# Kernel tuning notes

Measured on AMD Instinct MI355X. Metric: run time of the kernel, lower is better.

Reference implementation:

```python
import jax, jax.numpy as jnp
import numpy as np

N, D_IN, D_OUT, E = 16384, 2048, 2048, 8


def setup_inputs() -> dict:
    key = jax.random.key(0)
    k1, k2, k3, k4 = jax.random.split(key, 4)
    x = jax.random.normal(k1, (N, D_IN), dtype=jnp.float32)
    idxs = jax.random.randint(k2, (N,), 0, E, dtype=jnp.int64)
    # nn.Linear params: weight [out, in], bias [out]; stacked over experts.
    W = jax.random.normal(k3, (E, D_OUT, D_IN), dtype=jnp.float32) * (1.0 / np.sqrt(D_IN))
    b = jax.random.normal(k4, (E, D_OUT), dtype=jnp.float32) * 0.01
    return {"x": x, "idxs": idxs, "W": W, "b": b}


def reference(x, idxs, W, b):
    # Hard-routed MoE: each token goes to exactly one expert's Linear, then ReLU.
    # Loop over the small fixed expert count; each iteration is one dense GEMM
    # over all tokens, combined with a per-token routing mask (equivalent math
    # to the original masked gather/scatter since every token matches exactly
    # one expert id in [0, E)).
    n_experts = W.shape[0]
    y = jnp.zeros((x.shape[0], W.shape[1]), dtype=x.dtype)
    for e in range(n_experts):
        mask = (idxs == e)[:, None]  # [N, 1]
        y_e = x @ W[e].T + b[e]      # [N, out]
        y = jnp.where(mask, y_e, y)
    return jax.nn.relu(y)
```

## Files before the change

kernel.cpp:

```cpp
#include <hip/hip_runtime.h>
#include <stdint.h>

#define N_TOK 16384
#define D_IN  2048
#define D_OUT 2048
#define NEXP  8

#define BM 256
#define BN 128
#define BK 32
#define NKT (D_IN / BK)
#define NX4 (N_TOK * D_IN / 4)
#define NW4 (NEXP * D_OUT * D_IN / 4)

typedef __attribute__((ext_vector_type(8))) short bf16x8;
typedef __attribute__((ext_vector_type(4))) float f32x4;
typedef __attribute__((ext_vector_type(4))) unsigned short u16x4;

static __device__ __forceinline__ unsigned short f2bf(float x) {
  unsigned u = __builtin_bit_cast(unsigned, x);
  u += 0x7FFFu + ((u >> 16) & 1u);
  return (unsigned short)(u >> 16);
}
static __device__ __forceinline__ float bf2f(unsigned short h) {
  unsigned u = ((unsigned)h) << 16;
  return __builtin_bit_cast(float, u);
}

__global__ void zero_cnt(int* cnt) {
  if (threadIdx.x < NEXP) cnt[threadIdx.x] = 0;
}

__global__ void route_kernel(const int* __restrict__ idxs, int* __restrict__ cnt,
                             int* __restrict__ bucket) {
  __shared__ int hist[NEXP];
  __shared__ int base[NEXP];
  __shared__ int pos[NEXP];
  const int t = blockIdx.x * 256 + threadIdx.x;
  if (threadIdx.x < NEXP) { hist[threadIdx.x] = 0; pos[threadIdx.x] = 0; }
  __syncthreads();
  const int e = idxs[t];
  atomicAdd(&hist[e], 1);
  __syncthreads();
  if (threadIdx.x < NEXP)
    base[threadIdx.x] = atomicAdd(&cnt[threadIdx.x], hist[threadIdx.x]);
  __syncthreads();
  const int r = atomicAdd(&pos[e], 1);
  bucket[e * N_TOK + base[e] + r] = t;
}

__global__ void split_both(const float* __restrict__ x, const float* __restrict__ W,
                           unsigned short* __restrict__ xhi, unsigned short* __restrict__ xlo,
                           unsigned short* __restrict__ whi, unsigned short* __restrict__ wlo) {
  const int total = NX4 + NW4;
  for (int i = blockIdx.x * blockDim.x + threadIdx.x; i < total; i += gridDim.x * blockDim.x) {
    const bool isx = (i < NX4);
    const int j = isx ? i : i - NX4;
    const float4 v = isx ? ((const float4*)x)[j] : ((const float4*)W)[j];
    float f[4] = {v.x, v.y, v.z, v.w};
    u16x4 h, l;
#pragma unroll
    for (int k = 0; k < 4; ++k) {
      unsigned short hh = f2bf(f[k]);
      h[k] = hh;
      l[k] = f2bf(f[k] - bf2f(hh));
    }
    unsigned short* dh = (isx ? xhi : whi) + (size_t)j * 4;
    unsigned short* dl = (isx ? xlo : wlo) + (size_t)j * 4;
    *(u16x4*)dh = h;
    *(u16x4*)dl = l;
  }
}

#define GLD16(g, l)                                                                    \
  __builtin_amdgcn_global_load_lds((const __attribute__((address_space(1))) void*)(g), \
                                   (__attribute__((address_space(3))) void*)(l), 16, 0, 0)
#define SB() __builtin_amdgcn_sched_barrier(0)
#define BAR() __builtin_amdgcn_s_barrier()

__global__ __launch_bounds__(512)
void moe_gemm(const unsigned short* __restrict__ xhi, const unsigned short* __restrict__ xlo,
              const unsigned short* __restrict__ whi, const unsigned short* __restrict__ wlo,
              const float* __restrict__ bias, const int* __restrict__ cnt,
              const int* __restrict__ bucket, float* __restrict__ out) {
  const int bid = blockIdx.x;
  const int e = bid & 7;
  const int rem = bid >> 3;
  const int my = rem >> 4;
  const int nb = rem & 15;
  const int count = cnt[e];
  const int m0 = my * BM;
  if (m0 >= count) return;
  const int n0 = nb * BN;

  __shared__ __align__(16) char sbuf[3][49152];
  __shared__ int rowtok[BM];

  const int tid = threadIdx.x;
  const int lane = tid & 63;
  const int w = tid >> 6;
  const int wrM = (w >> 1) * 64;
  const int wcN = (w & 1) * 64;

  if (tid < BM) {
    int r = m0 + tid;
    rowtok[tid] = bucket[e * N_TOK + (r < count ? r : count - 1)];
  }
  __syncthreads();

  const unsigned short* whiE = whi + (size_t)e * D_OUT * D_IN;
  const unsigned short* wloE = wlo + (size_t)e * D_OUT * D_IN;
  const unsigned short* srcb[6];
  {
    const int g = tid >> 3;
    const int c = (tid & 7) ^ (g & 7);
    const int half = c >> 2, kc = c & 3;
#pragma unroll
    for (int q = 0; q < 4; ++q) {
      const int tok = rowtok[q * 64 + g];
      srcb[q] = (half ? xlo : xhi) + (size_t)tok * D_IN + kc * 8;
    }
#pragma unroll
    for (int q = 0; q < 2; ++q) {
      srcb[4 + q] = (half ? wloE : whiE) + (size_t)(n0 + q * 64 + g) * D_IN + kc * 8;
    }
  }
  const int dstw = w * 1024;

  const int off0 = (lane & 15) * 128 + (((lane >> 4) ^ (lane & 7)) * 16);

  f32x4 acc[4][4];
#pragma unroll
  for (int i = 0; i < 4; ++i)
#pragma unroll
    for (int j = 0; j < 4; ++j) acc[i][j] = (f32x4)0.0f;

#pragma unroll
  for (int q = 0; q < 4; ++q) GLD16(srcb[q], sbuf[0] + q * 8192 + dstw);
#pragma unroll
  for (int q = 0; q < 2; ++q) GLD16(srcb[4 + q], sbuf[0] + 32768 + q * 8192 + dstw);
#pragma unroll
  for (int q = 0; q < 4; ++q) GLD16(srcb[q] + BK, sbuf[1] + q * 8192 + dstw);
#pragma unroll
  for (int q = 0; q < 2; ++q) GLD16(srcb[4 + q] + BK, sbuf[1] + 32768 + q * 8192 + dstw);
  SB();
  asm volatile("s_waitcnt vmcnt(6)" ::: "memory");
  BAR(); SB();

#define COMPUTE(rb)                                                              \
  {                                                                              \
    bf16x8 ah[4], al[4], bh[4], bl[4];                                           \
    _Pragma("unroll") for (int m = 0; m < 4; ++m) {                              \
      const char* p = (rb) + (wrM + m * 16) * 128;                               \
      ah[m] = *(const bf16x8*)(p + off0);                                        \
      al[m] = *(const bf16x8*)(p + (off0 ^ 64));                                 \
    }                                                                            \
    _Pragma("unroll") for (int n = 0; n < 4; ++n) {                              \
      const char* p = (rb) + 32768 + (wcN + n * 16) * 128;                       \
      bh[n] = *(const bf16x8*)(p + off0);                                        \
      bl[n] = *(const bf16x8*)(p + (off0 ^ 64));                                 \
    }                                                                            \
    __builtin_amdgcn_s_setprio(1);                                               \
    _Pragma("unroll") for (int m = 0; m < 4; ++m)                                \
    _Pragma("unroll") for (int n = 0; n < 4; ++n) {                              \
      f32x4 a = acc[m][n];                                                       \
      a = __builtin_amdgcn_mfma_f32_16x16x32_bf16(ah[m], bh[n], a, 0, 0, 0);     \
      a = __builtin_amdgcn_mfma_f32_16x16x32_bf16(ah[m], bl[n], a, 0, 0, 0);     \
      a = __builtin_amdgcn_mfma_f32_16x16x32_bf16(al[m], bh[n], a, 0, 0, 0);     \
      acc[m][n] = a;                                                             \
    }                                                                            \
    __builtin_amdgcn_s_setprio(0);                                               \
  }

  int i = 0;
  for (; i < NKT - 2; ++i) {
    const char* rb = sbuf[i % 3];
    char* wb = sbuf[(i + 2) % 3];
    const int kt = (i + 2) * BK;
#pragma unroll
    for (int q = 0; q < 4; ++q) GLD16(srcb[q] + kt, wb + q * 8192 + dstw);
#pragma unroll
    for (int q = 0; q < 2; ++q) GLD16(srcb[4 + q] + kt, wb + 32768 + q * 8192 + dstw);
    SB();
    COMPUTE(rb);
    SB();
    asm volatile("s_waitcnt vmcnt(6)" ::: "memory");
    BAR(); SB();
  }
  {
    const char* rb = sbuf[i % 3];
    COMPUTE(rb);
    SB();
    asm volatile("s_waitcnt vmcnt(0)" ::: "memory");
    BAR(); SB();
    ++i;
  }
  {
    const char* rb = sbuf[i % 3];
    COMPUTE(rb);
  }

  const int r16 = lane & 15;
  const int rb4 = (lane >> 4) * 4;
#pragma unroll
  for (int n = 0; n < 4; ++n) {
    const int gn = n0 + wcN + n * 16 + r16;
    const float bv = bias[e * D_OUT + gn];
#pragma unroll
    for (int m = 0; m < 4; ++m) {
      const int lr = wrM + m * 16 + rb4;
#pragma unroll
      for (int i2 = 0; i2 < 4; ++i2) {
        const int row = lr + i2;
        if (m0 + row < count) {
          out[(size_t)rowtok[row] * D_OUT + gn] = fmaxf(acc[m][n][i2] + bv, 0.0f);
        }
      }
    }
  }
#undef COMPUTE
}

__global__ void fallback_kernel(const float* __restrict__ x, const int* __restrict__ idxs,
                                const float* __restrict__ W, const float* __restrict__ b,
                                float* __restrict__ out) {
  const int row = blockIdx.y;
  const int col = blockIdx.x * 256 + threadIdx.x;
  const int e = idxs[row];
  const float4* xr = (const float4*)(x + (size_t)row * D_IN);
  const float4* wr = (const float4*)(W + ((size_t)e * D_OUT + col) * D_IN);
  float acc = 0.f;
  for (int k = 0; k < D_IN / 4; ++k) {
    float4 a = xr[k], w = wr[k];
    acc += a.x * w.x + a.y * w.y + a.z * w.z + a.w * w.w;
  }
  out[(size_t)row * D_OUT + col] = fmaxf(acc + b[e * D_OUT + col], 0.0f);
}

extern "C" void kernel_launch(void* const* d_in, const int* in_sizes, int n_in,
                              void* d_out, int out_size, void* d_ws, size_t ws_size,
                              hipStream_t stream) {
  const float* x = (const float*)d_in[0];
  const int* idxs = (const int*)d_in[1];
  const float* W = (const float*)d_in[2];
  const float* b = (const float*)d_in[3];
  float* out = (float*)d_out;

  size_t off = 0;
  auto alloc = [&](size_t bytes) {
    void* p = (char*)d_ws + off;
    off += (bytes + 255) & ~(size_t)255;
    return p;
  };
  int* cnt = (int*)alloc(NEXP * sizeof(int));
  int* bucket = (int*)alloc((size_t)NEXP * N_TOK * sizeof(int));
  unsigned short* xhi = (unsigned short*)alloc((size_t)N_TOK * D_IN * 2);
  unsigned short* xlo = (unsigned short*)alloc((size_t)N_TOK * D_IN * 2);
  unsigned short* whi = (unsigned short*)alloc((size_t)NEXP * D_OUT * D_IN * 2);
  unsigned short* wlo = (unsigned short*)alloc((size_t)NEXP * D_OUT * D_IN * 2);

  if (off > ws_size) {
    dim3 g(D_OUT / 256, N_TOK, 1);
    fallback_kernel<<<g, 256, 0, stream>>>(x, idxs, W, b, out);
    return;
  }

  zero_cnt<<<1, 64, 0, stream>>>(cnt);
  route_kernel<<<N_TOK / 256, 256, 0, stream>>>(idxs, cnt, bucket);
  split_both<<<2048, 256, 0, stream>>>(x, W, xhi, xlo, whi, wlo);

  const int nblk = NEXP * (N_TOK / BM) * (D_OUT / BN);
  moe_gemm<<<nblk, 512, 0, stream>>>(xhi, xlo, whi, wlo, b, cnt, bucket, out);
}
```

Before: 953.6 us.

## Enlarge GEMM tile to 256x256 and switch to double-buffered LDS pipeline

Doubles the N tile from 128 to 256 so each 256-row block of x is reused across twice as many output columns, halving redundant A-tile loads per output. Waves are rearranged into a 2x4 grid, each computing 128x64 in two M-halves with a 32-entry accumulator array. The triple-buffered prefetch-two-ahead pipeline becomes a double-buffered prefetch-one-ahead loop with extra barriers per iteration. This raises register and LDS pressure and gives less latency hiding in exchange for better data reuse.

```diff
diff --git a/kernel.cpp b/kernel.cpp
--- a/kernel.cpp
+++ b/kernel.cpp
@@ -7,7 +7,7 @@
 #define NEXP  8
 
 #define BM 256
-#define BN 128
+#define BN 256
 #define BK 32
 #define NKT (D_IN / BK)
 #define NX4 (N_TOK * D_IN / 4)
@@ -86,21 +86,21 @@
   const int bid = blockIdx.x;
   const int e = bid & 7;
   const int rem = bid >> 3;
-  const int my = rem >> 4;
-  const int nb = rem & 15;
+  const int my = rem >> 3;
+  const int nb = rem & 7;
   const int count = cnt[e];
   const int m0 = my * BM;
   if (m0 >= count) return;
   const int n0 = nb * BN;
 
-  __shared__ __align__(16) char sbuf[3][49152];
+  __shared__ __align__(16) char sbuf[2][65536];
   __shared__ int rowtok[BM];
 
   const int tid = threadIdx.x;
   const int lane = tid & 63;
   const int w = tid >> 6;
-  const int wrM = (w >> 1) * 64;
-  const int wcN = (w & 1) * 64;
+  const int wr = w >> 2;
+  const int wc = w & 3;
 
   if (tid < BM) {
     int r = m0 + tid;
@@ -110,7 +110,7 @@
 
   const unsigned short* whiE = whi + (size_t)e * D_OUT * D_IN;
   const unsigned short* wloE = wlo + (size_t)e * D_OUT * D_IN;
-  const unsigned short* srcb[6];
+  const unsigned short* srcb[8];
   {
     const int g = tid >> 3;
     const int c = (tid & 7) ^ (g & 7);
@@ -121,7 +121,7 @@
       srcb[q] = (half ? xlo : xhi) + (size_t)tok * D_IN + kc * 8;
     }
 #pragma unroll
-    for (int q = 0; q < 2; ++q) {
+    for (int q = 0; q < 4; ++q) {
       srcb[4 + q] = (half ? wloE : whiE) + (size_t)(n0 + q * 64 + g) * D_IN + kc * 8;
     }
   }
@@ -129,86 +129,74 @@
 
   const int off0 = (lane & 15) * 128 + (((lane >> 4) ^ (lane & 7)) * 16);
 
-  f32x4 acc[4][4];
-#pragma unroll
-  for (int i = 0; i < 4; ++i)
+  f32x4 acc[8][4];
+#pragma unroll
+  for (int i = 0; i < 8; ++i)
 #pragma unroll
     for (int j = 0; j < 4; ++j) acc[i][j] = (f32x4)0.0f;
 
 #pragma unroll
-  for (int q = 0; q < 4; ++q) GLD16(srcb[q], sbuf[0] + q * 8192 + dstw);
-#pragma unroll
-  for (int q = 0; q < 2; ++q) GLD16(srcb[4 + q], sbuf[0] + 32768 + q * 8192 + dstw);
-#pragma unroll
-  for (int q = 0; q < 4; ++q) GLD16(srcb[q] + BK, sbuf[1] + q * 8192 + dstw);
-#pragma unroll
-  for (int q = 0; q < 2; ++q) GLD16(srcb[4 + q] + BK, sbuf[1] + 32768 + q * 8192 + dstw);
-  SB();
-  asm volatile("s_waitcnt vmcnt(6)" ::: "memory");
-  BAR(); SB();
-
-#define COMPUTE(rb)                                                              \
-  {                                                                              \
-    bf16x8 ah[4], al[4], bh[4], bl[4];                                           \
-    _Pragma("unroll") for (int m = 0; m < 4; ++m) {                              \
-      const char* p = (rb) + (wrM + m * 16) * 128;                               \
-      ah[m] = *(const bf16x8*)(p + off0);                                        \
-      al[m] = *(const bf16x8*)(p + (off0 ^ 64));                                 \
-    }                                                                            \
-    _Pragma("unroll") for (int n = 0; n < 4; ++n) {                              \
-      const char* p = (rb) + 32768 + (wcN + n * 16) * 128;                       \
-      bh[n] = *(const bf16x8*)(p + off0);                                        \
-      bl[n] = *(const bf16x8*)(p + (off0 ^ 64));                                 \
-    }                                                                            \
-    __builtin_amdgcn_s_setprio(1);                                               \
-    _Pragma("unroll") for (int m = 0; m < 4; ++m)                                \
-    _Pragma("unroll") for (int n = 0; n < 4; ++n) {                              \
-      f32x4 a = acc[m][n];                                                       \
-      a = __builtin_amdgcn_mfma_f32_16x16x32_bf16(ah[m], bh[n], a, 0, 0, 0);     \
-      a = __builtin_amdgcn_mfma_f32_16x16x32_bf16(ah[m], bl[n], a, 0, 0, 0);     \
-      a = __builtin_amdgcn_mfma_f32_16x16x32_bf16(al[m], bh[n], a, 0, 0, 0);     \
-      acc[m][n] = a;                                                             \
-    }                                                                            \
-    __builtin_amdgcn_s_setprio(0);                                               \
-  }
-
-  int i = 0;
-  for (; i < NKT - 2; ++i) {
-    const char* rb = sbuf[i % 3];
-    char* wb = sbuf[(i + 2) % 3];
-    const int kt = (i + 2) * BK;
-#pragma unroll
-    for (int q = 0; q < 4; ++q) GLD16(srcb[q] + kt, wb + q * 8192 + dstw);
-#pragma unroll
-    for (int q = 0; q < 2; ++q) GLD16(srcb[4 + q] + kt, wb + 32768 + q * 8192 + dstw);
+  for (int q = 0; q < 8; ++q)
+    GLD16(srcb[q], sbuf[0] + (q < 4 ? 0 : 32768) + (q & 3) * 8192 + dstw);
+
+  for (int i = 0; i < NKT; ++i) {
+    const char* rb = sbuf[i & 1];
+    char* wb = sbuf[(i + 1) & 1];
+
+    BAR();
     SB();
-    COMPUTE(rb);
+    if (i + 1 < NKT) {
+      const int kt = (i + 1) * BK;
+#pragma unroll
+      for (int q = 0; q < 8; ++q)
+        GLD16(srcb[q] + kt, wb + (q < 4 ? 0 : 32768) + (q & 3) * 8192 + dstw);
+      asm volatile("s_waitcnt vmcnt(8)" ::: "memory");
+    } else {
+      asm volatile("s_waitcnt vmcnt(0)" ::: "memory");
+    }
+    BAR();
     SB();
-    asm volatile("s_waitcnt vmcnt(6)" ::: "memory");
-    BAR(); SB();
-  }
-  {
-    const char* rb = sbuf[i % 3];
-    COMPUTE(rb);
-    SB();
-    asm volatile("s_waitcnt vmcnt(0)" ::: "memory");
-    BAR(); SB();
-    ++i;
-  }
-  {
-    const char* rb = sbuf[i % 3];
-    COMPUTE(rb);
+
+#pragma unroll
+    for (int mh = 0; mh < 2; ++mh) {
+      bf16x8 ah[4], al[4], bh[4], bl[4];
+#pragma unroll
+      for (int mf = 0; mf < 4; ++mf) {
+        const char* p = rb + (wr * 128 + mh * 64 + mf * 16) * 128;
+        ah[mf] = *(const bf16x8*)(p + off0);
+        al[mf] = *(const bf16x8*)(p + (off0 ^ 64));
+      }
+#pragma unroll
+      for (int nf = 0; nf < 4; ++nf) {
+        const char* p = rb + 32768 + (wc * 64 + nf * 16) * 128;
+        bh[nf] = *(const bf16x8*)(p + off0);
+        bl[nf] = *(const bf16x8*)(p + (off0 ^ 64));
+      }
+      __builtin_amdgcn_s_setprio(1);
+#pragma unroll
+      for (int mf = 0; mf < 4; ++mf)
+#pragma unroll
+        for (int nf = 0; nf < 4; ++nf) {
+          f32x4 a = acc[mh * 4 + mf][nf];
+          a = __builtin_amdgcn_mfma_f32_16x16x32_bf16(ah[mf], bh[nf], a, 0, 0, 0);
+          a = __builtin_amdgcn_mfma_f32_16x16x32_bf16(ah[mf], bl[nf], a, 0, 0, 0);
+          a = __builtin_amdgcn_mfma_f32_16x16x32_bf16(al[mf], bh[nf], a, 0, 0, 0);
+          acc[mh * 4 + mf][nf] = a;
+        }
+      __builtin_amdgcn_s_setprio(0);
+      if (mh == 0) { BAR(); }
+    }
   }
 
   const int r16 = lane & 15;
   const int rb4 = (lane >> 4) * 4;
 #pragma unroll
   for (int n = 0; n < 4; ++n) {
-    const int gn = n0 + wcN + n * 16 + r16;
+    const int gn = n0 + wc * 64 + n * 16 + r16;
     const float bv = bias[e * D_OUT + gn];
 #pragma unroll
-    for (int m = 0; m < 4; ++m) {
-      const int lr = wrM + m * 16 + rb4;
+    for (int m = 0; m < 8; ++m) {
+      const int lr = wr * 128 + m * 16 + rb4;
 #pragma unroll
       for (int i2 = 0; i2 < 4; ++i2) {
         const int row = lr + i2;
@@ -218,7 +206,6 @@
       }
     }
   }
-#undef COMPUTE
 }
 
 __global__ void fallback_kernel(const float* __restrict__ x, const int* __restrict__ idxs,
```

Result: faster. 898.8 us (-5.7%).
